# Kernel optimization log

Hardware: AMD Instinct MI355X
Metric: run time of the kernel (lower is better)

The kernel has to match this reference:

```python
import jax, jax.numpy as jnp
import numpy as np

B, C, O = 32, 32, 64
H = W_IN = 64
K = 3
OH = H - K + 1   # 62
OW = W_IN - K + 1  # 62


def setup_inputs() -> dict:
    key = jax.random.key(0)
    k1, k2 = jax.random.split(key)
    x = jax.random.normal(k1, (B, C, H, W_IN), dtype=jnp.float32)
    # per-position unshared weights: (out_ch, in_ch, out_h, out_w, K, K)
    weights = jax.random.normal(k2, (O, C, OH, OW, K, K), dtype=jnp.float32)
    biases = jnp.zeros((O, OH, OW), dtype=jnp.float32)
    return {"x": x, "weights": weights, "biases": biases}


def reference(x, weights, biases):
    # Extract all KxK patches with static slices (im2col), shape (B,C,OH,OW,K,K)
    patches = jnp.stack(
        [jnp.stack([x[:, :, ki:ki + OH, kj:kj + OW] for kj in range(K)], axis=-1)
         for ki in range(K)], axis=-2)
    # Per-position contraction over (c, ku, kv); weights unshared across (i, j)
    out = jnp.einsum('bcijuv,ocijuv->boij', patches, weights) + biases[None]
    return out
```

## Files before the change

### kernel.cpp

```cpp
#include <hip/hip_runtime.h>


#define B_  32
#define C_  32
#define O_  64
#define H_  64
#define W_  64
#define K_  3
#define OH_ 62
#define OW_ 62

#define OSTR  (C_ * OH_ * OW_ * K_ * K_)
#define CSTRW (OH_ * OW_ * K_ * K_)
#define BSTRX (C_ * H_ * W_)
#define CSTRX (H_ * W_)

typedef float f4 __attribute__((ext_vector_type(4)));

__global__ __launch_bounds__(256, 2)
void lcl_fwd(const float* __restrict__ x, const float* __restrict__ w,
             const float* __restrict__ bias, float* __restrict__ out) {
    __shared__ float wlds[2][4][OW_][12];

    const int j  = threadIdx.x & 63;
    const int wv = threadIdx.x >> 6;
    const int i  = blockIdx.y;
    const int ob = blockIdx.x * 4;
    const int b0 = wv * 8;
    const bool act = (j < OW_);

    float acc[8][4];
#pragma unroll
    for (int b = 0; b < 8; ++b)
#pragma unroll
        for (int o = 0; o < 4; ++o) acc[b][o] = 0.0f;

    const float* wrec0 = w + ((size_t)((ob + wv) * C_) * OH_ + i) * OW_ * 9 + (size_t)j * 9;
    const int jm1 = (j == 0) ? 0 : (j - 1);

    if (act) {
        const float* p = wrec0;
        f4 a, b;
        __builtin_memcpy(&a, p, 16);
        __builtin_memcpy(&b, p + 4, 16);
        *(f4*)&wlds[0][wv][j][0] = a;
        *(f4*)&wlds[0][wv][j][4] = b;
        wlds[0][wv][j][8] = p[8];
    }
    __syncthreads();

    for (int c = 0; c < C_; ++c) {
        const int cur = c & 1;
        const bool st = act && (c + 1 < C_);

        f4 sa, sb; float sc8 = 0.0f;
        if (st) {
            const float* p = wrec0 + (size_t)(c + 1) * CSTRW;
            __builtin_memcpy(&sa, p, 16);
            __builtin_memcpy(&sb, p + 4, 16);
            sc8 = p[8];
        }

        if (act) {
            float wt[4][9];
#pragma unroll
            for (int o = 0; o < 4; ++o) {
                f4 a = *(const f4*)&wlds[cur][o][j][0];
                f4 b = *(const f4*)&wlds[cur][o][j][4];
                wt[o][0] = a.x; wt[o][1] = a.y; wt[o][2] = a.z; wt[o][3] = a.w;
                wt[o][4] = b.x; wt[o][5] = b.y; wt[o][6] = b.z; wt[o][7] = b.w;
                wt[o][8] = wlds[cur][o][j][8];
            }

            const float* xrow0 = x + ((size_t)(b0 * C_ + c) * CSTRX) + (size_t)i * W_ + jm1;
#pragma unroll
            for (int b = 0; b < 8; ++b) {
                const float* xb = xrow0 + (size_t)b * BSTRX;
#pragma unroll
                for (int u = 0; u < K_; ++u) {
                    f4 xr;
                    __builtin_memcpy(&xr, xb + u * W_, 16);
                    const float x0 = (j == 0) ? xr.x : xr.y;
                    const float x1 = (j == 0) ? xr.y : xr.z;
                    const float x2 = (j == 0) ? xr.z : xr.w;
#pragma unroll
                    for (int o = 0; o < 4; ++o) {
                        acc[b][o] = fmaf(x0, wt[o][u * 3 + 0], acc[b][o]);
                        acc[b][o] = fmaf(x1, wt[o][u * 3 + 1], acc[b][o]);
                        acc[b][o] = fmaf(x2, wt[o][u * 3 + 2], acc[b][o]);
                    }
                }
            }
        }

        if (st) {
            const int nxt = cur ^ 1;
            *(f4*)&wlds[nxt][wv][j][0] = sa;
            *(f4*)&wlds[nxt][wv][j][4] = sb;
            wlds[nxt][wv][j][8] = sc8;
        }
        __syncthreads();
    }

    if (act) {
        const int pos = i * OW_ + j;
        float bz[4];
#pragma unroll
        for (int o = 0; o < 4; ++o) bz[o] = bias[(ob + o) * (OH_ * OW_) + pos];

#pragma unroll
        for (int b = 0; b < 8; ++b) {
#pragma unroll
            for (int o = 0; o < 4; ++o) {
                out[(((size_t)(b0 + b) * O_ + (ob + o)) * OH_ + i) * OW_ + j] = acc[b][o] + bz[o];
            }
        }
    }
}

extern "C" void kernel_launch(void* const* d_in, const int* in_sizes, int n_in,
                              void* d_out, int out_size, void* d_ws, size_t ws_size,
                              hipStream_t stream) {
    const float* x    = (const float*)d_in[0];
    const float* w    = (const float*)d_in[1];
    const float* bias = (const float*)d_in[2];
    float* out = (float*)d_out;

    dim3 grid(O_ / 4, OH_);
    dim3 block(256);
    lcl_fwd<<<grid, block, 0, stream>>>(x, w, bias, out);
}
```

Measured before the change: 595.5 us.

## Double block to 512 threads with 4 batches per wave and transposed LDS weights

Each block now runs 8 waves, each covering 4 batch elements instead of 8, so per-thread accumulator and register pressure are halved and more waves are resident to hide latency. Only the first 4 waves stage weights into LDS. The LDS weight tile is transposed to [o][tap][j], giving conflict-free scalar reads instead of strided vector reads. The cost is that every weight is reused across half as many batch elements per thread, and more waves take part in each barrier.

```diff
diff --git a/kernel.cpp b/kernel.cpp
--- a/kernel.cpp
+++ b/kernel.cpp
@@ -10,48 +10,50 @@
 #define OH_ 62
 #define OW_ 62
 
-#define OSTR  (C_ * OH_ * OW_ * K_ * K_)
 #define CSTRW (OH_ * OW_ * K_ * K_)
 #define BSTRX (C_ * H_ * W_)
 #define CSTRX (H_ * W_)
 
 typedef float f4 __attribute__((ext_vector_type(4)));
 
-__global__ __launch_bounds__(256, 2)
+__global__ __launch_bounds__(512, 2)
 void lcl_fwd(const float* __restrict__ x, const float* __restrict__ w,
              const float* __restrict__ bias, float* __restrict__ out) {
-    __shared__ float wlds[2][4][OW_][12];
+    __shared__ float wlds[2][4][9][64];
 
     const int j  = threadIdx.x & 63;
     const int wv = threadIdx.x >> 6;
     const int i  = blockIdx.y;
     const int ob = blockIdx.x * 4;
-    const int b0 = wv * 8;
+    const int b0 = wv * 4;
     const bool act = (j < OW_);
+    const bool stg = act && (wv < 4);
 
-    float acc[8][4];
+    float acc[4][4];
 #pragma unroll
-    for (int b = 0; b < 8; ++b)
+    for (int b = 0; b < 4; ++b)
 #pragma unroll
         for (int o = 0; o < 4; ++o) acc[b][o] = 0.0f;
 
-    const float* wrec0 = w + ((size_t)((ob + wv) * C_) * OH_ + i) * OW_ * 9 + (size_t)j * 9;
+    const float* wrec0 = w + ((size_t)((ob + (wv & 3)) * C_) * OH_ + i) * OW_ * 9 + (size_t)j * 9;
     const int jm1 = (j == 0) ? 0 : (j - 1);
 
-    if (act) {
+    if (stg) {
         const float* p = wrec0;
         f4 a, b;
         __builtin_memcpy(&a, p, 16);
         __builtin_memcpy(&b, p + 4, 16);
-        *(f4*)&wlds[0][wv][j][0] = a;
-        *(f4*)&wlds[0][wv][j][4] = b;
-        wlds[0][wv][j][8] = p[8];
+        wlds[0][wv][0][j] = a.x; wlds[0][wv][1][j] = a.y;
+        wlds[0][wv][2][j] = a.z; wlds[0][wv][3][j] = a.w;
+        wlds[0][wv][4][j] = b.x; wlds[0][wv][5][j] = b.y;
+        wlds[0][wv][6][j] = b.z; wlds[0][wv][7][j] = b.w;
+        wlds[0][wv][8][j] = p[8];
     }
     __syncthreads();
 
     for (int c = 0; c < C_; ++c) {
         const int cur = c & 1;
-        const bool st = act && (c + 1 < C_);
+        const bool st = stg && (c + 1 < C_);
 
         f4 sa, sb; float sc8 = 0.0f;
         if (st) {
@@ -64,20 +66,16 @@
         if (act) {
             float wt[4][9];
 #pragma unroll
-            for (int o = 0; o < 4; ++o) {
-                f4 a = *(const f4*)&wlds[cur][o][j][0];
-                f4 b = *(const f4*)&wlds[cur][o][j][4];
-                wt[o][0] = a.x; wt[o][1] = a.y; wt[o][2] = a.z; wt[o][3] = a.w;
-                wt[o][4] = b.x; wt[o][5] = b.y; wt[o][6] = b.z; wt[o][7] = b.w;
-                wt[o][8] = wlds[cur][o][j][8];
-            }
+            for (int o = 0; o < 4; ++o)
+#pragma unroll
+                for (int t = 0; t < 9; ++t) wt[o][t] = wlds[cur][o][t][j];
 
             const float* xrow0 = x + ((size_t)(b0 * C_ + c) * CSTRX) + (size_t)i * W_ + jm1;
 #pragma unroll
-            for (int b = 0; b < 8; ++b) {
+            for (int b = 0; b < 4; ++b) {
                 const float* xb = xrow0 + (size_t)b * BSTRX;
 #pragma unroll
-                for (int u = 0; u < K_; ++u) {
+                for (int u = 0; u < 3; ++u) {
                     f4 xr;
                     __builtin_memcpy(&xr, xb + u * W_, 16);
                     const float x0 = (j == 0) ? xr.x : xr.y;
@@ -95,9 +93,11 @@
 
         if (st) {
             const int nxt = cur ^ 1;
-            *(f4*)&wlds[nxt][wv][j][0] = sa;
-            *(f4*)&wlds[nxt][wv][j][4] = sb;
-            wlds[nxt][wv][j][8] = sc8;
+            wlds[nxt][wv][0][j] = sa.x; wlds[nxt][wv][1][j] = sa.y;
+            wlds[nxt][wv][2][j] = sa.z; wlds[nxt][wv][3][j] = sa.w;
+            wlds[nxt][wv][4][j] = sb.x; wlds[nxt][wv][5][j] = sb.y;
+            wlds[nxt][wv][6][j] = sb.z; wlds[nxt][wv][7][j] = sb.w;
+            wlds[nxt][wv][8][j] = sc8;
         }
         __syncthreads();
     }
@@ -109,7 +109,7 @@
         for (int o = 0; o < 4; ++o) bz[o] = bias[(ob + o) * (OH_ * OW_) + pos];
 
 #pragma unroll
-        for (int b = 0; b < 8; ++b) {
+        for (int b = 0; b < 4; ++b) {
 #pragma unroll
             for (int o = 0; o < 4; ++o) {
                 out[(((size_t)(b0 + b) * O_ + (ob + o)) * OH_ + i) * OW_ + j] = acc[b][o] + bz[o];
@@ -127,6 +127,6 @@
     float* out = (float*)d_out;
 
     dim3 grid(O_ / 4, OH_);
-    dim3 block(256);
+    dim3 block(512);
     lcl_fwd<<<grid, block, 0, stream>>>(x, w, bias, out);
 }
```

Result: faster. 484.6 us (-18.6%).
